# Performance work log

Hardware: AMD Instinct MI355X
Metric: run time of the kernel (lower is better)

Reference implementation:

```python
import jax, jax.numpy as jnp
import numpy as np
import math

IN_DIM = 256
OUT_DIM = 256
HEADS = 4
D_K = OUT_DIM // HEADS


def setup_inputs() -> dict:
    key = jax.random.key(0)
    ks = jax.random.split(key, 10)
    B, N = 4, 4096
    x = jax.random.normal(ks[0], (B, N, IN_DIM), dtype=jnp.float32)
    adj = jax.random.randint(ks[1], (B, N, N), 0, 2, dtype=jnp.int32)
    s = 1.0 / math.sqrt(IN_DIM)
    Wq = jax.random.normal(ks[2], (IN_DIM, OUT_DIM), dtype=jnp.float32) * s
    bq = jnp.zeros((OUT_DIM,), dtype=jnp.float32)
    Wk = jax.random.normal(ks[3], (IN_DIM, OUT_DIM), dtype=jnp.float32) * s
    bk = jnp.zeros((OUT_DIM,), dtype=jnp.float32)
    Wv = jax.random.normal(ks[4], (IN_DIM, OUT_DIM), dtype=jnp.float32) * s
    bv = jnp.zeros((OUT_DIM,), dtype=jnp.float32)
    Wo = jax.random.normal(ks[5], (OUT_DIM, OUT_DIM), dtype=jnp.float32) * (1.0 / math.sqrt(OUT_DIM))
    bo = jnp.zeros((OUT_DIM,), dtype=jnp.float32)
    return {"x": x, "adj": adj, "Wq": Wq, "bq": bq, "Wk": Wk, "bk": bk,
            "Wv": Wv, "bv": bv, "Wo": Wo, "bo": bo}


def reference(x, adj, Wq, bq, Wk, bk, Wv, bv, Wo, bo):
    B, N, _ = x.shape
    q = (x @ Wq + bq).reshape(B, N, HEADS, D_K)
    k = (x @ Wk + bk).reshape(B, N, HEADS, D_K)
    v = (x @ Wv + bv).reshape(B, N, HEADS, D_K)
    scale = 1.0 / math.sqrt(D_K + 1e-9)
    scores = jnp.einsum('bnhd,bmhd->bhnm', q, k) * scale  # [B,H,N,N]
    eye = jnp.eye(N, dtype=bool)
    mask = (adj.astype(bool) | eye)[:, None, :, :]  # [B,1,N,N]
    min_val = jnp.finfo(scores.dtype).min
    scores = jnp.where(mask, scores, min_val)
    attn = jax.nn.softmax(scores, axis=-1)
    out = jnp.einsum('bhnm,bmhd->bnhd', attn, v).reshape(B, N, OUT_DIM)
    out = out @ Wo + bo
    return jax.nn.relu(out)
```

## Files before the change

kernel.cpp:

```cpp
#include <hip/hip_runtime.h>
#include <hip/hip_bf16.h>

#define DI 256
#define DOUT 256
#define NH 4
#define NB 4
#define NN 4096

typedef __attribute__((ext_vector_type(8))) short bf16x8;
typedef __attribute__((ext_vector_type(4))) float f32x4;
typedef __attribute__((ext_vector_type(4))) unsigned short u16x4;
typedef __attribute__((ext_vector_type(8))) unsigned short u16x8;

#define MFMA16(a, b, c) __builtin_amdgcn_mfma_f32_16x16x32_bf16((a), (b), (c), 0, 0, 0)

#define SCALE_L2E 0.18033688011112043f
#define DEFER_THR 8.0f

static __device__ __forceinline__ unsigned short f2bf(float f) {
  union { __hip_bfloat16 h; unsigned short u; } c;
  c.h = __float2bfloat16(f);
  return c.u;
}

static __device__ __forceinline__ void gl_lds16(const void* g, void* l) {
  __builtin_amdgcn_global_load_lds(
      (const __attribute__((address_space(1))) void*)g,
      (__attribute__((address_space(3))) void*)l, 16, 0, 0);
}

__global__ __launch_bounds__(256) void k_cvt_x(const float* __restrict__ x,
                                               unsigned short* __restrict__ xb) {
  int i = blockIdx.x * 256 + threadIdx.x;
  float4 v = ((const float4*)x)[i];
  u16x4 o;
  o[0] = f2bf(v.x); o[1] = f2bf(v.y); o[2] = f2bf(v.z); o[3] = f2bf(v.w);
  ((u16x4*)xb)[i] = o;
}

__global__ __launch_bounds__(256) void k_cvt_w(
    const float* __restrict__ Wq, const float* __restrict__ Wk,
    const float* __restrict__ Wv, const float* __restrict__ Wo,
    unsigned short* __restrict__ wtq, unsigned short* __restrict__ wtk,
    unsigned short* __restrict__ wtv, unsigned short* __restrict__ wto) {
  int t = blockIdx.x * 256 + threadIdx.x;
  int m = t >> 13, k0 = ((t >> 8) & 31) * 8, n = t & 255;
  const float* W = (m == 0) ? Wq : (m == 1) ? Wk : (m == 2) ? Wv : Wo;
  unsigned short* dst = (m == 0) ? wtq : (m == 1) ? wtk : (m == 2) ? wtv : wto;
  u16x8 o;
#pragma unroll
  for (int j = 0; j < 8; ++j) o[j] = f2bf(W[(k0 + j) * 256 + n]);
  *(u16x8*)(dst + n * 256 + k0) = o;
}

__global__ __launch_bounds__(256) void k_pack(const int* __restrict__ adj,
                                              unsigned long long* __restrict__ pm) {
  const int gw = blockIdx.x * 4 + (threadIdx.x >> 6);
  const int l = threadIdx.x & 63;
  const int b = gw >> 15, c = (gw >> 9) & 63, n0 = (gw & 511) << 3;
  unsigned long long myb = 0;
#pragma unroll
  for (int j = 0; j < 8; ++j) {
    int a = adj[((size_t)b * NN + n0 + j) * NN + c * 64 + l];
    unsigned long long bal = __ballot(a != 0);
    if (l == j) myb = bal;
  }
  if (l < 8) pm[((size_t)b * 64 + c) * NN + n0 + l] = myb;
}

__global__ __launch_bounds__(256) void k_proj(
    const unsigned short* __restrict__ xb,
    const unsigned short* __restrict__ wtq, const unsigned short* __restrict__ wtk,
    const unsigned short* __restrict__ wtv,
    const float* __restrict__ bq, const float* __restrict__ bk, const float* __restrict__ bv,
    unsigned short* __restrict__ qh, unsigned short* __restrict__ kh,
    unsigned short* __restrict__ vtb) {
  const int tid = threadIdx.x, w = tid >> 6, l = tid & 63, ql = l & 15, g = l >> 4;
  const int wz = blockIdx.z;
  const unsigned short* wt = (wz == 0) ? wtq : (wz == 1 ? wtk : wtv);
  const float* bias = (wz == 0) ? bq : (wz == 1 ? bk : bv);
  const int node0 = blockIdx.x * 64, nout0 = blockIdx.y * 64;
  const int wn = w >> 1, wm = w & 1;

  const unsigned short* a0 = wt + (size_t)(nout0 + 32 * wn + ql) * 256 + g * 8;
  const unsigned short* b0 = xb + (size_t)(node0 + 32 * wm + ql) * 256 + g * 8;

  f32x4 acc[2][2] = {};
#pragma unroll
  for (int kk = 0; kk < 256; kk += 32) {
    bf16x8 af0 = *(const bf16x8*)(a0 + kk);
    bf16x8 af1 = *(const bf16x8*)(a0 + 16 * 256 + kk);
    bf16x8 bf0 = *(const bf16x8*)(b0 + kk);
    bf16x8 bf1 = *(const bf16x8*)(b0 + 16 * 256 + kk);
    acc[0][0] = MFMA16(af0, bf0, acc[0][0]);
    acc[0][1] = MFMA16(af0, bf1, acc[0][1]);
    acc[1][0] = MFMA16(af1, bf0, acc[1][0]);
    acc[1][1] = MFMA16(af1, bf1, acc[1][1]);
  }
  const int h = blockIdx.y;
  const float sc = (wz == 0) ? SCALE_L2E : 1.0f;
#pragma unroll
  for (int tn = 0; tn < 2; ++tn) {
    const int d0 = 32 * wn + 16 * tn + 4 * g;
    float bi[4];
#pragma unroll
    for (int r = 0; r < 4; ++r) bi[r] = bias[nout0 + d0 + r];
#pragma unroll
    for (int tm = 0; tm < 2; ++tm) {
      const int node = node0 + 32 * wm + 16 * tm + ql;
      const int b = node >> 12, n = node & 4095;
      if (wz < 2) {
        unsigned short* dst = (wz == 0 ? qh : kh) +
            ((size_t)(b * NH + h) * NN + n) * 64 + d0;
        u16x4 pk;
#pragma unroll
        for (int r = 0; r < 4; ++r) pk[r] = f2bf((acc[tn][tm][r] + bi[r]) * sc);
        *(u16x4*)dst = pk;
      } else {
#pragma unroll
        for (int r = 0; r < 4; ++r) {
          vtb[((size_t)(b * NH + h) * 64 + d0 + r) * NN + n] =
              f2bf(acc[tn][tm][r] + bi[r]);
        }
      }
    }
  }
}

__global__ __launch_bounds__(256, 4) void k_attn(
    const unsigned short* __restrict__ qh, const unsigned short* __restrict__ kh,
    const unsigned short* __restrict__ vtb, const unsigned long long* __restrict__ pm,
    unsigned short* __restrict__ aout) {
  const int tid = threadIdx.x, w = tid >> 6, l = tid & 63, ql = l & 15, g = l >> 4;
  const int n0 = blockIdx.x * 64, b = blockIdx.y, h = blockIdx.z;
  const int nq = n0 + 16 * w + ql;

  const unsigned short* qbase = qh + ((size_t)(b * NH + h) * NN + n0 + 16 * w) * 64;
  const char* kg = (const char*)(kh + (size_t)(b * NH + h) * NN * 64);
  const char* vg = (const char*)(vtb + (size_t)(b * NH + h) * 64 * NN);
  const unsigned long long* pmrow = pm + (size_t)b * 64 * NN + nq;

  __shared__ __align__(16) unsigned short kst[2][4096];
  __shared__ __align__(16) unsigned short vst[2][4096];
  __shared__ __align__(16) unsigned short plds[4][1024];

  bf16x8 qf0 = *(const bf16x8*)(qbase + ql * 64 + g * 8);
  bf16x8 qf1 = *(const bf16x8*)(qbase + ql * 64 + 32 + g * 8);

  const int swzc = ((l & 7) << 4) ^ ((l >> 3) << 4);
  const int lk = ((l >> 3) << 7) + swzc;
  const int lv = (l >> 3) * (NN * 2) + swzc;
  const int i0 = 2 * w, i1 = 2 * w + 1;
  char* klds = (char*)kst;
  char* vlds = (char*)vst;

#define STAGE(B, T)                                                              \
  do {                                                                           \
    gl_lds16(kg + (size_t)(T) * 8192 + i0 * 1024 + lk, klds + (B) * 8192 + i0 * 1024); \
    gl_lds16(kg + (size_t)(T) * 8192 + i1 * 1024 + lk, klds + (B) * 8192 + i1 * 1024); \
    gl_lds16(vg + (size_t)(T) * 128 + (size_t)i0 * (8 * NN * 2) + lv,            \
             vlds + (B) * 8192 + i0 * 1024);                                     \
    gl_lds16(vg + (size_t)(T) * 128 + (size_t)i1 * (8 * NN * 2) + lv,            \
             vlds + (B) * 8192 + i1 * 1024);                                     \
  } while (0)

  float mrun = -1e30f, lrun = 0.f;
  f32x4 oacc[4] = {};
  const int swz = (ql & 7) << 4;
  char* prow = (char*)&plds[w][0] + ql * 128;

  STAGE(0, 0);
  unsigned long long rm_cur = pmrow[0];
  unsigned long long rm_next = 0;
  __syncthreads();

  int buf = 0;
  for (int t = 0; t < NN / 64; ++t) {
    if (t < NN / 64 - 1) {
      STAGE(buf ^ 1, t + 1);
      rm_next = pmrow[(size_t)(t + 1) * NN];
    }
    f32x4 s[4];
    const char* kb = klds + buf * 8192;
#pragma unroll
    for (int t4 = 0; t4 < 4; ++t4) {
      const char* kr = kb + (16 * t4 + ql) * 128;
      bf16x8 kf0 = *(const bf16x8*)(kr + ((g * 16) ^ swz));
      bf16x8 kf1 = *(const bf16x8*)(kr + ((64 + g * 16) ^ swz));
      f32x4 z = {};
      z = MFMA16(kf0, qf0, z);
      s[t4] = MFMA16(kf1, qf1, z);
    }
    unsigned long long rm = rm_cur;
    const int dg = nq - (t << 6);
    if (dg >= 0 && dg < 64) rm |= (1ull << dg);
    float sv[16];
    float mx = -__builtin_inff();
#pragma unroll
    for (int t4 = 0; t4 < 4; ++t4)
#pragma unroll
      for (int r = 0; r < 4; ++r) {
        const int idx = 16 * t4 + 4 * g + r;
        float vv = ((rm >> idx) & 1ull) ? s[t4][r] : -__builtin_inff();
        sv[4 * t4 + r] = vv;
        mx = fmaxf(mx, vv);
      }
    mx = fmaxf(mx, __shfl_xor(mx, 16));
    mx = fmaxf(mx, __shfl_xor(mx, 32));
    if (!__all(mx <= mrun + DEFER_THR)) {
      const float mnew = fmaxf(mrun, mx);
      const float fsc = exp2f(mrun - mnew);
      lrun *= fsc;
#pragma unroll
      for (int u = 0; u < 4; ++u)
#pragma unroll
        for (int r = 0; r < 4; ++r) oacc[u][r] *= fsc;
      mrun = mnew;
    }
    float ls = 0.f;
#pragma unroll
    for (int t4 = 0; t4 < 4; ++t4) {
      u16x4 pk;
#pragma unroll
      for (int r = 0; r < 4; ++r) {
        float p = exp2f(sv[4 * t4 + r] - mrun);
        ls += p;
        pk[r] = f2bf(p);
      }
      *(u16x4*)(prow + ((32 * t4 + 8 * g) ^ swz)) = pk;
    }
    ls += __shfl_xor(ls, 16);
    ls += __shfl_xor(ls, 32);
    lrun += ls;
    bf16x8 pf0 = *(const bf16x8*)(prow + ((g * 16) ^ swz));
    bf16x8 pf1 = *(const bf16x8*)(prow + ((64 + g * 16) ^ swz));
    const char* vb = vlds + buf * 8192;
#pragma unroll
    for (int u = 0; u < 4; ++u) {
      const char* vr = vb + (16 * u + ql) * 128;
      bf16x8 vf0 = *(const bf16x8*)(vr + ((g * 16) ^ swz));
      bf16x8 vf1 = *(const bf16x8*)(vr + ((64 + g * 16) ^ swz));
      oacc[u] = MFMA16(vf0, pf0, oacc[u]);
      oacc[u] = MFMA16(vf1, pf1, oacc[u]);
    }
    __syncthreads();
    buf ^= 1;
    rm_cur = rm_next;
  }
#undef STAGE

  const float inv = 1.f / lrun;
  unsigned short* obase = aout + ((size_t)b * NN + nq) * DOUT + h * 64;
#pragma unroll
  for (int u = 0; u < 4; ++u) {
    u16x4 pk;
#pragma unroll
    for (int r = 0; r < 4; ++r) pk[r] = f2bf(oacc[u][r] * inv);
    *(u16x4*)(obase + 16 * u + 4 * g) = pk;
  }
}

__global__ __launch_bounds__(256) void k_oproj(
    const unsigned short* __restrict__ aout, const unsigned short* __restrict__ wto,
    const float* __restrict__ bo, float* __restrict__ out) {
  const int tid = threadIdx.x, w = tid >> 6, l = tid & 63, ql = l & 15, g = l >> 4;
  const int node0 = blockIdx.x * 64, nout0 = blockIdx.y * 64;
  const int wm = w & 1, wn = w >> 1;
  const unsigned short* a0 = aout + (size_t)(node0 + 32 * wm + ql) * 256 + g * 8;
  const unsigned short* b0 = wto + (size_t)(nout0 + 32 * wn + ql) * 256 + g * 8;

  f32x4 acc[2][2] = {};
#pragma unroll
  for (int kk = 0; kk < 256; kk += 32) {
    bf16x8 af0 = *(const bf16x8*)(a0 + kk);
    bf16x8 af1 = *(const bf16x8*)(a0 + 16 * 256 + kk);
    bf16x8 bf0 = *(const bf16x8*)(b0 + kk);
    bf16x8 bf1 = *(const bf16x8*)(b0 + 16 * 256 + kk);
    acc[0][0] = MFMA16(af0, bf0, acc[0][0]);
    acc[0][1] = MFMA16(af0, bf1, acc[0][1]);
    acc[1][0] = MFMA16(af1, bf0, acc[1][0]);
    acc[1][1] = MFMA16(af1, bf1, acc[1][1]);
  }
  float bi[2];
  bi[0] = bo[nout0 + 32 * wn + ql];
  bi[1] = bo[nout0 + 32 * wn + 16 + ql];
#pragma unroll
  for (int tm = 0; tm < 2; ++tm) {
    const int nodeb = node0 + 32 * wm + 16 * tm + 4 * g;
#pragma unroll
    for (int tn = 0; tn < 2; ++tn) {
      const int nout = nout0 + 32 * wn + 16 * tn + ql;
#pragma unroll
      for (int r = 0; r < 4; ++r) {
        float v = acc[tm][tn][r] + bi[tn];
        out[(size_t)(nodeb + r) * 256 + nout] = fmaxf(v, 0.f);
      }
    }
  }
}

extern "C" void kernel_launch(void* const* d_in, const int* in_sizes, int n_in,
                              void* d_out, int out_size, void* d_ws, size_t ws_size,
                              hipStream_t stream) {
  const float* x  = (const float*)d_in[0];
  const int*   adj = (const int*)d_in[1];
  const float* Wq = (const float*)d_in[2];
  const float* bq = (const float*)d_in[3];
  const float* Wk = (const float*)d_in[4];
  const float* bk = (const float*)d_in[5];
  const float* Wv = (const float*)d_in[6];
  const float* bv = (const float*)d_in[7];
  const float* Wo = (const float*)d_in[8];
  const float* bo = (const float*)d_in[9];
  float* out = (float*)d_out;

  unsigned short* ws = (unsigned short*)d_ws;
  const size_t NX = (size_t)NB * NN * DI;
  unsigned short* xb  = ws;
  unsigned short* wtq = xb + NX;
  unsigned short* wtk = wtq + 65536;
  unsigned short* wtv = wtk + 65536;
  unsigned short* wto = wtv + 65536;
  unsigned short* qhb = wto + 65536;
  unsigned short* khb = qhb + NX;
  unsigned short* vtb = khb + NX;
  unsigned short* aout = xb;
  unsigned long long* pmask = (unsigned long long*)d_out;

  k_cvt_x<<<(int)(NX / 4 / 256), 256, 0, stream>>>(x, xb);
  k_cvt_w<<<128, 256, 0, stream>>>(Wq, Wk, Wv, Wo, wtq, wtk, wtv, wto);
  k_pack<<<32768, 256, 0, stream>>>(adj, pmask);
  dim3 gp(NB * NN / 64, 4, 3);
  k_proj<<<gp, 256, 0, stream>>>(xb, wtq, wtk, wtv, bq, bk, bv, qhb, khb, vtb);
  dim3 ga(NN / 64, NB, NH);
  k_attn<<<ga, 256, 0, stream>>>(qhb, khb, vtb, pmask, aout);
  dim3 go(NB * NN / 64, 4);
  k_oproj<<<go, 256, 0, stream>>>(aout, wto, bo, out);
}
```

Before: 618.5 us.

## Rework attention with 32x32 MFMA tiles, register P shuffle and no running max

Rewrites the attention kernel so each block handles 128 queries, with 32 queries per wave. It uses 32x32x16 bf16 MFMAs for both QK^T and PV, and keeps the probabilities in registers by packing them with v_cvt_pk_bf16_f32 and exchanging half-waves through shuffles instead of an LDS round trip. The online-softmax running max and rescaling are removed and exp2 is applied to the raw scaled scores, which avoids the max reduction and rescale work but can overflow if scores get large. The projection kernel now stages the transposed V tile in LDS so it can write coalesced 16-byte rows instead of scattered 2-byte stores. Occupancy is lowered to 2 blocks per SM via launch bounds.

After: 589.0 us. -4.8%, faster.

```diff
diff --git a/kernel.cpp b/kernel.cpp
--- a/kernel.cpp
+++ b/kernel.cpp
@@ -9,13 +9,14 @@
 
 typedef __attribute__((ext_vector_type(8))) short bf16x8;
 typedef __attribute__((ext_vector_type(4))) float f32x4;
+typedef __attribute__((ext_vector_type(16))) float f32x16;
 typedef __attribute__((ext_vector_type(4))) unsigned short u16x4;
 typedef __attribute__((ext_vector_type(8))) unsigned short u16x8;
 
 #define MFMA16(a, b, c) __builtin_amdgcn_mfma_f32_16x16x32_bf16((a), (b), (c), 0, 0, 0)
+#define MFMA32(a, b, c) __builtin_amdgcn_mfma_f32_32x32x16_bf16((a), (b), (c), 0, 0, 0)
 
 #define SCALE_L2E 0.18033688011112043f
-#define DEFER_THR 8.0f
 
 static __device__ __forceinline__ unsigned short f2bf(float f) {
   union { __hip_bfloat16 h; unsigned short u; } c;
@@ -82,6 +83,8 @@
   const int node0 = blockIdx.x * 64, nout0 = blockIdx.y * 64;
   const int wn = w >> 1, wm = w & 1;
 
+  __shared__ __align__(16) unsigned short vstage[64][64];
+
   const unsigned short* a0 = wt + (size_t)(nout0 + 32 * wn + ql) * 256 + g * 8;
   const unsigned short* b0 = xb + (size_t)(node0 + 32 * wm + ql) * 256 + g * 8;
 
@@ -118,58 +121,69 @@
         *(u16x4*)dst = pk;
       } else {
 #pragma unroll
-        for (int r = 0; r < 4; ++r) {
-          vtb[((size_t)(b * NH + h) * 64 + d0 + r) * NN + n] =
-              f2bf(acc[tn][tm][r] + bi[r]);
-        }
+        for (int r = 0; r < 4; ++r)
+          vstage[d0 + r][32 * wm + 16 * tm + ql] = f2bf(acc[tn][tm][r] + bi[r]);
       }
     }
   }
-}
-
-__global__ __launch_bounds__(256, 4) void k_attn(
+  if (wz == 2) {
+    __syncthreads();
+    const int row = tid >> 2, ch = (tid & 3) * 16;
+    const int bb = node0 >> 12, nn0 = node0 & 4095;
+    unsigned short* dst = vtb + ((size_t)(bb * NH + h) * 64 + row) * NN + nn0 + ch;
+    *(u16x8*)dst       = *(const u16x8*)&vstage[row][ch];
+    *(u16x8*)(dst + 8) = *(const u16x8*)&vstage[row][ch + 8];
+  }
+}
+
+__global__ __launch_bounds__(256, 2) void k_attn(
     const unsigned short* __restrict__ qh, const unsigned short* __restrict__ kh,
     const unsigned short* __restrict__ vtb, const unsigned long long* __restrict__ pm,
     unsigned short* __restrict__ aout) {
-  const int tid = threadIdx.x, w = tid >> 6, l = tid & 63, ql = l & 15, g = l >> 4;
-  const int n0 = blockIdx.x * 64, b = blockIdx.y, h = blockIdx.z;
-  const int nq = n0 + 16 * w + ql;
-
-  const unsigned short* qbase = qh + ((size_t)(b * NH + h) * NN + n0 + 16 * w) * 64;
+  const int tid = threadIdx.x, w = tid >> 6, l = tid & 63;
+  const int lq = l & 31, hi = l >> 5;
+  const int qb = blockIdx.x * 128, b = blockIdx.y, h = blockIdx.z;
+  const int nq = qb + 32 * w + lq;
+
+  const unsigned short* qbase = qh + ((size_t)(b * NH + h) * NN + qb + 32 * w) * 64;
   const char* kg = (const char*)(kh + (size_t)(b * NH + h) * NN * 64);
   const char* vg = (const char*)(vtb + (size_t)(b * NH + h) * 64 * NN);
   const unsigned long long* pmrow = pm + (size_t)b * 64 * NN + nq;
 
-  __shared__ __align__(16) unsigned short kst[2][4096];
-  __shared__ __align__(16) unsigned short vst[2][4096];
-  __shared__ __align__(16) unsigned short plds[4][1024];
-
-  bf16x8 qf0 = *(const bf16x8*)(qbase + ql * 64 + g * 8);
-  bf16x8 qf1 = *(const bf16x8*)(qbase + ql * 64 + 32 + g * 8);
-
-  const int swzc = ((l & 7) << 4) ^ ((l >> 3) << 4);
-  const int lk = ((l >> 3) << 7) + swzc;
-  const int lv = (l >> 3) * (NN * 2) + swzc;
-  const int i0 = 2 * w, i1 = 2 * w + 1;
-  char* klds = (char*)kst;
-  char* vlds = (char*)vst;
-
-#define STAGE(B, T)                                                              \
-  do {                                                                           \
-    gl_lds16(kg + (size_t)(T) * 8192 + i0 * 1024 + lk, klds + (B) * 8192 + i0 * 1024); \
-    gl_lds16(kg + (size_t)(T) * 8192 + i1 * 1024 + lk, klds + (B) * 8192 + i1 * 1024); \
-    gl_lds16(vg + (size_t)(T) * 128 + (size_t)i0 * (8 * NN * 2) + lv,            \
-             vlds + (B) * 8192 + i0 * 1024);                                     \
-    gl_lds16(vg + (size_t)(T) * 128 + (size_t)i1 * (8 * NN * 2) + lv,            \
-             vlds + (B) * 8192 + i1 * 1024);                                     \
+  __shared__ __align__(16) char kst[2][8192];
+  __shared__ __align__(16) char vst[2][8192];
+  __shared__ float llds[4][32];
+
+  bf16x8 qf[4];
+#pragma unroll
+  for (int ds = 0; ds < 4; ++ds)
+    qf[ds] = *(const bf16x8*)(qbase + lq * 64 + ds * 16 + hi * 8);
+
+  const char* sp[4];
+  int doff[4];
+  const int widx = (w & 1) * 4;
+#pragma unroll
+  for (int j = 0; j < 4; ++j) {
+    const int idx = widx + j;
+    const int tt = idx >> 2, cc = idx & 3;
+    sp[j] = (w < 2) ? (kg + (size_t)(32 * tt + lq) * 128 + cc * 32 + hi * 16)
+                    : (vg + (size_t)(32 * tt + lq) * (2 * NN) + cc * 32 + hi * 16);
+    doff[j] = idx * 1024;
+  }
+  char* dbase = (w < 2) ? (char*)kst : (char*)vst;
+  const long sinc = (w < 2) ? 8192 : 128;
+
+#define STAGE(B)                                              \
+  do {                                                        \
+    _Pragma("unroll") for (int j = 0; j < 4; ++j)             \
+        gl_lds16(sp[j], dbase + (B) * 8192 + doff[j]);        \
+    _Pragma("unroll") for (int j = 0; j < 4; ++j) sp[j] += sinc; \
   } while (0)
 
-  float mrun = -1e30f, lrun = 0.f;
-  f32x4 oacc[4] = {};
-  const int swz = (ql & 7) << 4;
-  char* prow = (char*)&plds[w][0] + ql * 128;
-
-  STAGE(0, 0);
+  f32x16 oA = {}, oB = {};
+  float lrun = 0.f;
+
+  STAGE(0);
   unsigned long long rm_cur = pmrow[0];
   unsigned long long rm_next = 0;
   __syncthreads();
@@ -177,71 +191,60 @@
   int buf = 0;
   for (int t = 0; t < NN / 64; ++t) {
     if (t < NN / 64 - 1) {
-      STAGE(buf ^ 1, t + 1);
+      STAGE(buf ^ 1);
       rm_next = pmrow[(size_t)(t + 1) * NN];
     }
-    f32x4 s[4];
-    const char* kb = klds + buf * 8192;
-#pragma unroll
-    for (int t4 = 0; t4 < 4; ++t4) {
-      const char* kr = kb + (16 * t4 + ql) * 128;
-      bf16x8 kf0 = *(const bf16x8*)(kr + ((g * 16) ^ swz));
-      bf16x8 kf1 = *(const bf16x8*)(kr + ((64 + g * 16) ^ swz));
-      f32x4 z = {};
-      z = MFMA16(kf0, qf0, z);
-      s[t4] = MFMA16(kf1, qf1, z);
+    const char* kbuf = (const char*)kst + buf * 8192;
+    const char* vbuf = (const char*)vst + buf * 8192;
+    f32x16 s0 = {}, s1 = {};
+#pragma unroll
+    for (int ds = 0; ds < 4; ++ds) {
+      bf16x8 kf0 = *(const bf16x8*)(kbuf + ds * 1024 + l * 16);
+      bf16x8 kf1 = *(const bf16x8*)(kbuf + (4 + ds) * 1024 + l * 16);
+      s0 = MFMA32(kf0, qf[ds], s0);
+      s1 = MFMA32(kf1, qf[ds], s1);
     }
     unsigned long long rm = rm_cur;
     const int dg = nq - (t << 6);
     if (dg >= 0 && dg < 64) rm |= (1ull << dg);
-    float sv[16];
-    float mx = -__builtin_inff();
-#pragma unroll
-    for (int t4 = 0; t4 < 4; ++t4)
-#pragma unroll
-      for (int r = 0; r < 4; ++r) {
-        const int idx = 16 * t4 + 4 * g + r;
-        float vv = ((rm >> idx) & 1ull) ? s[t4][r] : -__builtin_inff();
-        sv[4 * t4 + r] = vv;
-        mx = fmaxf(mx, vv);
-      }
-    mx = fmaxf(mx, __shfl_xor(mx, 16));
-    mx = fmaxf(mx, __shfl_xor(mx, 32));
-    if (!__all(mx <= mrun + DEFER_THR)) {
-      const float mnew = fmaxf(mrun, mx);
-      const float fsc = exp2f(mrun - mnew);
-      lrun *= fsc;
-#pragma unroll
-      for (int u = 0; u < 4; ++u)
-#pragma unroll
-        for (int r = 0; r < 4; ++r) oacc[u][r] *= fsc;
-      mrun = mnew;
-    }
-    float ls = 0.f;
-#pragma unroll
-    for (int t4 = 0; t4 < 4; ++t4) {
-      u16x4 pk;
-#pragma unroll
-      for (int r = 0; r < 4; ++r) {
-        float p = exp2f(sv[4 * t4 + r] - mrun);
-        ls += p;
-        pk[r] = f2bf(p);
-      }
-      *(u16x4*)(prow + ((32 * t4 + 8 * g) ^ swz)) = pk;
-    }
-    ls += __shfl_xor(ls, 16);
-    ls += __shfl_xor(ls, 32);
-    lrun += ls;
-    bf16x8 pf0 = *(const bf16x8*)(prow + ((g * 16) ^ swz));
-    bf16x8 pf1 = *(const bf16x8*)(prow + ((64 + g * 16) ^ swz));
-    const char* vb = vlds + buf * 8192;
-#pragma unroll
-    for (int u = 0; u < 4; ++u) {
-      const char* vr = vb + (16 * u + ql) * 128;
-      bf16x8 vf0 = *(const bf16x8*)(vr + ((g * 16) ^ swz));
-      bf16x8 vf1 = *(const bf16x8*)(vr + ((64 + g * 16) ^ swz));
-      oacc[u] = MFMA16(vf0, pf0, oacc[u]);
-      oacc[u] = MFMA16(vf1, pf1, oacc[u]);
+    const unsigned long long rmh = rm >> (4 * hi);
+    unsigned pw0[8], pw1[8];
+#pragma unroll
+    for (int m = 0; m < 8; ++m) {
+      const int c = 2 * (m & 1) + 8 * (m >> 1);
+      float a0 = ((rmh >> c) & 1ull)        ? s0[2 * m]     : -__builtin_inff();
+      float a1 = ((rmh >> (c + 1)) & 1ull)  ? s0[2 * m + 1] : -__builtin_inff();
+      float c0 = ((rmh >> (c + 32)) & 1ull) ? s1[2 * m]     : -__builtin_inff();
+      float c1 = ((rmh >> (c + 33)) & 1ull) ? s1[2 * m + 1] : -__builtin_inff();
+      a0 = exp2f(a0);
+      a1 = exp2f(a1);
+      c0 = exp2f(c0);
+      c1 = exp2f(c1);
+      lrun += (a0 + a1) + (c0 + c1);
+      asm("v_cvt_pk_bf16_f32 %0, %1, %2" : "=v"(pw0[m]) : "v"(a0), "v"(a1));
+      asm("v_cvt_pk_bf16_f32 %0, %1, %2" : "=v"(pw1[m]) : "v"(c0), "v"(c1));
+    }
+    unsigned px0[8], px1[8];
+#pragma unroll
+    for (int m = 0; m < 8; ++m) {
+      px0[m] = (unsigned)__shfl_xor((int)pw0[m], 32);
+      px1[m] = (unsigned)__shfl_xor((int)pw1[m], 32);
+    }
+    union pf_u { unsigned u[4]; bf16x8 v; };
+#pragma unroll
+    for (int s = 0; s < 4; ++s) {
+      const unsigned* pw = (s < 2) ? pw0 : pw1;
+      const unsigned* px = (s < 2) ? px0 : px1;
+      const int o = (s & 1) * 4;
+      pf_u pp;
+      pp.u[0] = hi ? px[o + 2] : pw[o + 0];
+      pp.u[1] = hi ? px[o + 3] : pw[o + 1];
+      pp.u[2] = hi ? pw[o + 2] : px[o + 0];
+      pp.u[3] = hi ? pw[o + 3] : px[o + 1];
+      bf16x8 vfa = *(const bf16x8*)(vbuf + s * 1024 + l * 16);
+      bf16x8 vfb = *(const bf16x8*)(vbuf + (4 + s) * 1024 + l * 16);
+      oA = MFMA32(pp.v, vfa, oA);
+      oB = MFMA32(pp.v, vfb, oB);
     }
     __syncthreads();
     buf ^= 1;
@@ -249,14 +252,16 @@
   }
 #undef STAGE
 
-  const float inv = 1.f / lrun;
-  unsigned short* obase = aout + ((size_t)b * NN + nq) * DOUT + h * 64;
-#pragma unroll
-  for (int u = 0; u < 4; ++u) {
-    u16x4 pk;
-#pragma unroll
-    for (int r = 0; r < 4; ++r) pk[r] = f2bf(oacc[u][r] * inv);
-    *(u16x4*)(obase + 16 * u + 4 * g) = pk;
+  lrun += __shfl_xor(lrun, 32);
+  if (l < 32) llds[w][l] = 1.0f / lrun;
+  __syncthreads();
+#pragma unroll
+  for (int r = 0; r < 16; ++r) {
+    const int qloc = (r & 3) + 8 * (r >> 2) + 4 * hi;
+    const float inv = llds[w][qloc];
+    unsigned short* op = aout + ((size_t)b * NN + qb + 32 * w + qloc) * 256 + h * 64 + lq;
+    op[0]  = f2bf(oA[r] * inv);
+    op[32] = f2bf(oB[r] * inv);
   }
 }
 
@@ -332,7 +337,7 @@
   k_pack<<<32768, 256, 0, stream>>>(adj, pmask);
   dim3 gp(NB * NN / 64, 4, 3);
   k_proj<<<gp, 256, 0, stream>>>(xb, wtq, wtk, wtv, bq, bk, bv, qhb, khb, vtb);
-  dim3 ga(NN / 64, NB, NH);
+  dim3 ga(NN / 128, NB, NH);
   k_attn<<<ga, 256, 0, stream>>>(qhb, khb, vtb, pmask, aout);
   dim3 go(NB * NN / 64, 4);
   k_oproj<<<go, 256, 0, stream>>>(aout, wto, bo, out);
```
